# Kernel tuning notes

Measured on AMD Instinct MI355X. Metric: run time of the kernel, lower is better.

The kernel has to match this reference:

```python
import jax, jax.numpy as jnp
import numpy as np


def setup_inputs() -> dict:
    key = jax.random.key(0)
    k_x, k_g, k_fc, k_pj = jax.random.split(key, 4)
    B, T, C, H, E = 4, 2048, 1024, 2048, 8
    n_layer = 12
    x = jax.random.normal(k_x, (B, T, C), dtype=jnp.float32)
    w_gate = 0.02 * jax.random.normal(k_g, (C, E), dtype=jnp.float32)
    w_fc = 0.02 * jax.random.normal(k_fc, (C, H, E), dtype=jnp.float32)
    w_proj = (0.02 * (2 * n_layer) ** -0.5) * jax.random.normal(k_pj, (H, C, E), dtype=jnp.float32)
    return {"x": x, "w_gate": w_gate, "w_fc": w_fc, "w_proj": w_proj, "top_k": 2}


def reference(x, w_gate, w_fc, w_proj, top_k):
    # x: (B,T,C); w_gate: (C,E); w_fc: (C,H,E); w_proj: (H,C,E)
    E = w_gate.shape[-1]
    gate = jnp.einsum('btc,ce->bte', x, w_gate)                  # gating logits
    top_vals, top_idx = jax.lax.top_k(gate, top_k)               # (B,T,K) — raw logits used as combine weights (as in source)
    # Per-expert combine weight: sum_k top_val_k * onehot(idx_k) — zero for unselected experts.
    # This is mathematically identical to gathering the K expert weight slices per token
    # (the source's gather+einsum) but avoids the (B,T,C,H,K) weight blowup.
    onehot = jax.nn.one_hot(top_idx, E, dtype=x.dtype)           # (B,T,K,E)
    w_e = jnp.einsum('btk,btke->bte', top_vals, onehot)          # (B,T,E)
    h = jax.nn.silu(jnp.einsum('btc,che->bthe', x, w_fc))        # (B,T,H,E)
    o = jnp.einsum('bthe,bte,hce->btc', h, w_e, w_proj)          # weighted expert combine
    return o
```

## Files before the change

### kernel.cpp

```cpp
#include <hip/hip_runtime.h>
#include <hip/hip_bf16.h>


#define NTOK 8192
#define CD   1024
#define HD   2048
#define NE   8
#define NSLOT 16384
#define MTILES 20

typedef short  short4_t  __attribute__((ext_vector_type(4)));
typedef short  short8_t  __attribute__((ext_vector_type(8)));
typedef __bf16 bf16x8_t  __attribute__((ext_vector_type(8)));
typedef float  f32x4_t   __attribute__((ext_vector_type(4)));

struct FragArg {
  short8_t v;
  __device__ operator short8_t() const { return v; }
  __device__ operator bf16x8_t() const { return __builtin_bit_cast(bf16x8_t, v); }
};

static __device__ __forceinline__ float b2f(unsigned short u) {
  union { float f; unsigned int i; } w; w.i = ((unsigned int)u) << 16; return w.f;
}
static __device__ __forceinline__ unsigned short f2b(float f) {
  unsigned int u = __float_as_uint(f);
  u += 0x7fffu + ((u >> 16) & 1u);
  return (unsigned short)(u >> 16);
}
static __device__ __forceinline__ void gl2lds16(const void* g, void* l) {
  __builtin_amdgcn_global_load_lds((__attribute__((address_space(1))) void*)g,
                                   (__attribute__((address_space(3))) void*)l,
                                   16, 0, 0);
}
static __device__ __forceinline__ int swz(int row, int kc) {
  return row * 4 + (kc ^ ((row >> 1) & 3));
}

#define GATE_BLOCKS (NTOK / 4)
__global__ __launch_bounds__(256) void prep_kernel(
    const float* __restrict__ x, const float* __restrict__ wg,
    const float* __restrict__ wfc, const float* __restrict__ wpj,
    unsigned short* __restrict__ xb,
    unsigned short* __restrict__ wfcp, unsigned short* __restrict__ wpjp,
    int* __restrict__ tok_e, float* __restrict__ tok_v,
    int* __restrict__ g_counts)
{
  __shared__ __align__(16) unsigned short lds[NE * 32 * 40];
  __shared__ int hist[NE];
  int t = threadIdx.x;

  if (blockIdx.x < GATE_BLOCKS) {
    if (t < NE) hist[t] = 0;
    __syncthreads();
    int wv = t >> 6, lane = t & 63;
    int tk = blockIdx.x * 4 + wv;
    const float* xr = x + (size_t)tk * CD;
    unsigned short* xbr = xb + (size_t)tk * CD;
    float acc[NE] = {0, 0, 0, 0, 0, 0, 0, 0};
    #pragma unroll
    for (int jj = 0; jj < 4; ++jj) {
      int c0 = (lane + 64 * jj) * 4;
      float4 xv = *(const float4*)(xr + c0);
      short4_t ob;
      ob[0] = (short)f2b(xv.x); ob[1] = (short)f2b(xv.y);
      ob[2] = (short)f2b(xv.z); ob[3] = (short)f2b(xv.w);
      *(short4_t*)(xbr + c0) = ob;
      #pragma unroll
      for (int j = 0; j < 4; ++j) {
        float xf = (j == 0) ? xv.x : (j == 1) ? xv.y : (j == 2) ? xv.z : xv.w;
        const float* wr = wg + (size_t)(c0 + j) * NE;
        float4 w0 = *(const float4*)wr;
        float4 w1 = *(const float4*)(wr + 4);
        acc[0] += xf * w0.x; acc[1] += xf * w0.y;
        acc[2] += xf * w0.z; acc[3] += xf * w0.w;
        acc[4] += xf * w1.x; acc[5] += xf * w1.y;
        acc[6] += xf * w1.z; acc[7] += xf * w1.w;
      }
    }
    #pragma unroll
    for (int off = 32; off >= 1; off >>= 1)
      #pragma unroll
      for (int e = 0; e < NE; ++e) acc[e] += __shfl_down(acc[e], off, 64);
    if (lane == 0) {
      float v1 = -3.0e38f, v2 = -3.0e38f; int i1 = 0, i2 = 1;
      #pragma unroll
      for (int e = 0; e < NE; ++e) {
        float g = acc[e];
        if (g > v1) { v2 = v1; i2 = i1; v1 = g; i1 = e; }
        else if (g > v2) { v2 = g; i2 = e; }
      }
      tok_e[tk * 2] = i1; tok_e[tk * 2 + 1] = i2;
      tok_v[tk * 2] = v1; tok_v[tk * 2 + 1] = v2;
      atomicAdd(&hist[i1], 1); atomicAdd(&hist[i2], 1);
    }
    __syncthreads();
    if (t < NE && hist[t] > 0) atomicAdd(&g_counts[t], hist[t]);
  } else {
    int pid = blockIdx.x - GATE_BLOCKS;
    int tensor = pid >> 11;
    int rem = pid & 2047;
    int bx = rem & 63, by = rem >> 6;
    const float* in; unsigned short* out; int D0, D1, b0, b1;
    if (tensor == 0) { in = wfc; out = wfcp; D0 = CD; D1 = HD;
                       b1 = bx * 32; b0 = by * 32; }
    else             { in = wpj; out = wpjp; D0 = HD; D1 = CD;
                       b1 = by * 32; b0 = bx * 32; }
    int d1i = t & 31, d0q = t >> 5;
    #pragma unroll
    for (int r = 0; r < 4; ++r) {
      int d0i = d0q * 4 + r;
      const float* src = in + ((size_t)(b0 + d0i) * D1 + (b1 + d1i)) * NE;
      float4 v0 = *(const float4*)src;
      float4 v1 = *(const float4*)(src + 4);
      unsigned short* dst0 = &lds[d1i * 40 + d0i];
      dst0[0 * 32 * 40] = f2b(v0.x);
      dst0[1 * 32 * 40] = f2b(v0.y);
      dst0[2 * 32 * 40] = f2b(v0.z);
      dst0[3 * 32 * 40] = f2b(v0.w);
      dst0[4 * 32 * 40] = f2b(v1.x);
      dst0[5 * 32 * 40] = f2b(v1.y);
      dst0[6 * 32 * 40] = f2b(v1.z);
      dst0[7 * 32 * 40] = f2b(v1.w);
    }
    __syncthreads();
    int dchunk = t & 3, d1w = (t >> 2) & 31, ehalf = t >> 7;
    #pragma unroll
    for (int p = 0; p < 4; ++p) {
      int e = ehalf + 2 * p;
      short8_t v = *(const short8_t*)&lds[e * 32 * 40 + d1w * 40 + dchunk * 8];
      *(short8_t*)(out + ((size_t)e * D1 + (b1 + d1w)) * D0 + b0 + dchunk * 8) = v;
    }
  }
}

__global__ __launch_bounds__(256) void scatter_kernel(
    const int* __restrict__ tok_e, const float* __restrict__ tok_v,
    const int* __restrict__ g_counts, int* __restrict__ g_cursor,
    int* __restrict__ g_base,
    int* __restrict__ bucket_tok, float* __restrict__ bucket_v,
    int* __restrict__ slot_of)
{
  int gid = blockIdx.x * 256 + threadIdx.x;
  int lane = threadIdx.x & 63;
  int base[NE];
  { int o = 0;
    #pragma unroll
    for (int e = 0; e < NE; ++e) { base[e] = o; o += g_counts[e]; } }
  int e = tok_e[gid];
  unsigned long long lanebit = 1ull << lane;
  int pos = 0;
  #pragma unroll
  for (int ee = 0; ee < NE; ++ee) {
    unsigned long long m = __ballot(e == ee);
    if (e == ee) {
      int leader = __ffsll((long long)m) - 1;
      int cnt = __popcll(m);
      int start = 0;
      if (lane == leader) start = atomicAdd(&g_cursor[ee], cnt);
      start = __shfl(start, leader, 64);
      pos = start + __popcll(m & (lanebit - 1));
    }
  }
  int sl = base[e] + pos;
  bucket_tok[sl] = gid >> 1;
  bucket_v[sl]   = tok_v[gid];
  slot_of[gid]   = sl;
  if (gid < NE) g_base[gid] = base[gid];
}

__global__ __launch_bounds__(256) void gemm1_kernel(
    const unsigned short* __restrict__ xb, const unsigned short* __restrict__ wfcp,
    const int* __restrict__ g_counts, const int* __restrict__ g_base,
    const int* __restrict__ bucket_tok, const float* __restrict__ bucket_v,
    unsigned short* __restrict__ hbuf)
{
  int id = blockIdx.x;
  int xcd = id & 7;
  int r = id >> 3;
  int nt = r & 15;
  int g = (r >> 4) * 8 + xcd;
  int e = g / MTILES, mt = g % MTILES;

  int cnt = g_counts[e];
  int m0 = mt * 128;
  if (m0 >= cnt) return;
  int base = g_base[e];
  int n0 = nt * 128;

  __shared__ __align__(16) unsigned short lsA[128 * 32];
  __shared__ __align__(16) unsigned short lsB[128 * 32];
  __shared__ int   s_tok[128];
  __shared__ float s_v[128];

  int t = threadIdx.x;
  if (t < 128) {
    int ok = (m0 + t) < cnt;
    s_tok[t] = ok ? bucket_tok[base + m0 + t] : 0;
    s_v[t]   = ok ? bucket_v[base + m0 + t] : 0.0f;
  }
  __syncthreads();

  int slot = t & 3;
  int r0 = t >> 2, r1 = r0 + 64;
  int gc0 = slot ^ ((r0 >> 1) & 3);
  int gc1 = slot ^ ((r1 >> 1) & 3);
  const unsigned short* gA0 = xb + (size_t)s_tok[r0] * CD + gc0 * 8;
  const unsigned short* gA1 = xb + (size_t)s_tok[r1] * CD + gc1 * 8;
  const unsigned short* gB0 = wfcp + ((size_t)e * HD + n0 + r0) * CD + gc0 * 8;
  const unsigned short* gB1 = wfcp + ((size_t)e * HD + n0 + r1) * CD + gc1 * 8;
  unsigned short* lA0 = &lsA[(size_t)t * 8];
  unsigned short* lA1 = &lsA[(size_t)(256 + t) * 8];
  unsigned short* lB0 = &lsB[(size_t)t * 8];
  unsigned short* lB1 = &lsB[(size_t)(256 + t) * 8];

  int lane = t & 63, wv = t >> 6;
  int wm = (wv & 1) * 64, wn = (wv >> 1) * 64;
  int ml = lane & 15, kq = lane >> 4;

  f32x4_t acc[4][4];
  #pragma unroll
  for (int i = 0; i < 4; ++i)
    #pragma unroll
    for (int j = 0; j < 4; ++j) acc[i][j] = (f32x4_t){0.f, 0.f, 0.f, 0.f};

  for (int k0 = 0; k0 < CD; k0 += 32) {
    __syncthreads();
    gl2lds16(gA0 + k0, lA0);
    gl2lds16(gA1 + k0, lA1);
    gl2lds16(gB0 + k0, lB0);
    gl2lds16(gB1 + k0, lB1);
    __syncthreads();
    short8_t af[4], bfr[4];
    #pragma unroll
    for (int i = 0; i < 4; ++i) {
      af[i]  = *(const short8_t*)&lsA[swz(wm + i * 16 + ml, kq) * 8];
      bfr[i] = *(const short8_t*)&lsB[swz(wn + i * 16 + ml, kq) * 8];
    }
    #pragma unroll
    for (int i = 0; i < 4; ++i)
      #pragma unroll
      for (int j = 0; j < 4; ++j)
        acc[i][j] = __builtin_amdgcn_mfma_f32_16x16x32_bf16(
            FragArg{af[i]}, FragArg{bfr[j]}, acc[i][j], 0, 0, 0);
  }

  #pragma unroll
  for (int i = 0; i < 4; ++i) {
    int rb = wm + i * 16 + kq * 4;
    #pragma unroll
    for (int r2 = 0; r2 < 4; ++r2) {
      int row = rb + r2;
      if (m0 + row < cnt) {
        float v = s_v[row];
        size_t ro = (size_t)(base + m0 + row) * HD + n0;
        #pragma unroll
        for (int j = 0; j < 4; ++j) {
          float z = acc[i][j][r2];
          float val = v * (z / (1.0f + __expf(-z)));
          hbuf[ro + wn + j * 16 + ml] = f2b(val);
        }
      }
    }
  }
}

__global__ __launch_bounds__(256) void gemm2_kernel(
    const unsigned short* __restrict__ hbuf, const unsigned short* __restrict__ wpjp,
    const int* __restrict__ g_counts, const int* __restrict__ g_base,
    unsigned short* __restrict__ oslot)
{
  int id = blockIdx.x;
  int xcd = id & 7;
  int r = id >> 3;
  int nt = r & 7;
  int g = (r >> 3) * 8 + xcd;
  int e = g / MTILES, mt = g % MTILES;

  int cnt = g_counts[e];
  int m0 = mt * 128;
  if (m0 >= cnt) return;
  int base = g_base[e];
  int n0 = nt * 128;

  __shared__ __align__(16) unsigned short lsA[128 * 32];
  __shared__ __align__(16) unsigned short lsB[128 * 32];

  int t = threadIdx.x;
  int slot = t & 3;
  int r0 = t >> 2, r1 = r0 + 64;
  int gc0 = slot ^ ((r0 >> 1) & 3);
  int gc1 = slot ^ ((r1 >> 1) & 3);
  const unsigned short* gA0 = hbuf + (size_t)(base + m0 + r0) * HD + gc0 * 8;
  const unsigned short* gA1 = hbuf + (size_t)(base + m0 + r1) * HD + gc1 * 8;
  const unsigned short* gB0 = wpjp + ((size_t)e * CD + n0 + r0) * HD + gc0 * 8;
  const unsigned short* gB1 = wpjp + ((size_t)e * CD + n0 + r1) * HD + gc1 * 8;
  unsigned short* lA0 = &lsA[(size_t)t * 8];
  unsigned short* lA1 = &lsA[(size_t)(256 + t) * 8];
  unsigned short* lB0 = &lsB[(size_t)t * 8];
  unsigned short* lB1 = &lsB[(size_t)(256 + t) * 8];

  int lane = t & 63, wv = t >> 6;
  int wm = (wv & 1) * 64, wn = (wv >> 1) * 64;
  int ml = lane & 15, kq = lane >> 4;

  f32x4_t acc[4][4];
  #pragma unroll
  for (int i = 0; i < 4; ++i)
    #pragma unroll
    for (int j = 0; j < 4; ++j) acc[i][j] = (f32x4_t){0.f, 0.f, 0.f, 0.f};

  for (int k0 = 0; k0 < HD; k0 += 32) {
    __syncthreads();
    gl2lds16(gA0 + k0, lA0);
    gl2lds16(gA1 + k0, lA1);
    gl2lds16(gB0 + k0, lB0);
    gl2lds16(gB1 + k0, lB1);
    __syncthreads();
    short8_t af[4], bfr[4];
    #pragma unroll
    for (int i = 0; i < 4; ++i) {
      af[i]  = *(const short8_t*)&lsA[swz(wm + i * 16 + ml, kq) * 8];
      bfr[i] = *(const short8_t*)&lsB[swz(wn + i * 16 + ml, kq) * 8];
    }
    #pragma unroll
    for (int i = 0; i < 4; ++i)
      #pragma unroll
      for (int j = 0; j < 4; ++j)
        acc[i][j] = __builtin_amdgcn_mfma_f32_16x16x32_bf16(
            FragArg{af[i]}, FragArg{bfr[j]}, acc[i][j], 0, 0, 0);
  }

  #pragma unroll
  for (int i = 0; i < 4; ++i) {
    int rb = wm + i * 16 + kq * 4;
    #pragma unroll
    for (int r2 = 0; r2 < 4; ++r2) {
      int row = rb + r2;
      if (m0 + row < cnt) {
        size_t ro = (size_t)(base + m0 + row) * CD + n0;
        #pragma unroll
        for (int j = 0; j < 4; ++j)
          oslot[ro + wn + j * 16 + ml] = f2b(acc[i][j][r2]);
      }
    }
  }
}

__global__ __launch_bounds__(256) void combine_kernel(
    const unsigned short* __restrict__ oslot, const int* __restrict__ slot_of,
    float* __restrict__ out)
{
  int gid = blockIdx.x * 256 + threadIdx.x;
  int tk = gid >> 7;
  int ch = (gid & 127) * 8;
  int s0 = slot_of[tk * 2], s1 = slot_of[tk * 2 + 1];
  short8_t a = *(const short8_t*)(oslot + (size_t)s0 * CD + ch);
  short8_t b = *(const short8_t*)(oslot + (size_t)s1 * CD + ch);
  float* op = out + (size_t)tk * CD + ch;
  float4 o0, o1;
  o0.x = b2f((unsigned short)a[0]) + b2f((unsigned short)b[0]);
  o0.y = b2f((unsigned short)a[1]) + b2f((unsigned short)b[1]);
  o0.z = b2f((unsigned short)a[2]) + b2f((unsigned short)b[2]);
  o0.w = b2f((unsigned short)a[3]) + b2f((unsigned short)b[3]);
  o1.x = b2f((unsigned short)a[4]) + b2f((unsigned short)b[4]);
  o1.y = b2f((unsigned short)a[5]) + b2f((unsigned short)b[5]);
  o1.z = b2f((unsigned short)a[6]) + b2f((unsigned short)b[6]);
  o1.w = b2f((unsigned short)a[7]) + b2f((unsigned short)b[7]);
  *(float4*)op = o0;
  *(float4*)(op + 4) = o1;
}

extern "C" void kernel_launch(void* const* d_in, const int* in_sizes, int n_in,
                              void* d_out, int out_size, void* d_ws, size_t ws_size,
                              hipStream_t stream)
{
  const float* x   = (const float*)d_in[0];
  const float* wg  = (const float*)d_in[1];
  const float* wfc = (const float*)d_in[2];
  const float* wpj = (const float*)d_in[3];
  float* out = (float*)d_out;

  char* w = (char*)d_ws;
  unsigned short* wfcp  = (unsigned short*)w; w += (size_t)NE * HD * CD * 2;
  unsigned short* wpjp  = (unsigned short*)w; w += (size_t)NE * CD * HD * 2;
  unsigned short* xb    = (unsigned short*)w; w += (size_t)NTOK * CD * 2;
  unsigned short* hbuf  = (unsigned short*)w; w += (size_t)NSLOT * HD * 2;
  unsigned short* oslot = (unsigned short*)w; w += (size_t)NSLOT * CD * 2;
  int*   tok_e      = (int*)w;   w += NSLOT * 4;
  float* tok_v      = (float*)w; w += NSLOT * 4;
  int*   slot_of    = (int*)w;   w += NSLOT * 4;
  int*   bucket_tok = (int*)w;   w += NSLOT * 4;
  float* bucket_v   = (float*)w; w += NSLOT * 4;
  int*   g_counts   = (int*)w;   w += NE * 4;
  int*   g_cursor   = (int*)w;   w += NE * 4;
  int*   g_base     = (int*)w;   w += 256;

  hipMemsetAsync(g_counts, 0, 2 * NE * sizeof(int), stream);
  prep_kernel<<<GATE_BLOCKS + 4096, 256, 0, stream>>>(
      x, wg, wfc, wpj, xb, wfcp, wpjp, tok_e, tok_v, g_counts);
  scatter_kernel<<<NSLOT / 256, 256, 0, stream>>>(
      tok_e, tok_v, g_counts, g_cursor, g_base, bucket_tok, bucket_v, slot_of);
  gemm1_kernel<<<(HD / 128) * MTILES * NE, 256, 0, stream>>>(
      xb, wfcp, g_counts, g_base, bucket_tok, bucket_v, hbuf);
  gemm2_kernel<<<(CD / 128) * MTILES * NE, 256, 0, stream>>>(
      hbuf, wpjp, g_counts, g_base, oslot);
  combine_kernel<<<(NTOK * CD / 8) / 256, 256, 0, stream>>>(oslot, slot_of, out);
}
```

Before: 466.4 us.

## Double K-tile depth to 64 and remap grid so expert follows XCD index

Both expert GEMM kernels now stage 64-wide K slices in LDS instead of 32, with an 8-way XOR swizzle and a per-wave load mapping. This halves the number of barrier pairs per output tile and gives two MFMA sub-steps per sync. Block indexing also changes so the expert id is taken from the low three bits of the block id, tying each expert to one XCD so its weights stay in that die's L2. LDS use doubles per block, which may lower occupancy, and per-XCD load now depends on how many tokens each expert receives.

```diff
diff --git a/kernel.cpp b/kernel.cpp
--- a/kernel.cpp
+++ b/kernel.cpp
@@ -8,6 +8,7 @@
 #define NE   8
 #define NSLOT 16384
 #define MTILES 20
+#define BK   64
 
 typedef short  short4_t  __attribute__((ext_vector_type(4)));
 typedef short  short8_t  __attribute__((ext_vector_type(8)));
@@ -32,9 +33,6 @@
   __builtin_amdgcn_global_load_lds((__attribute__((address_space(1))) void*)g,
                                    (__attribute__((address_space(3))) void*)l,
                                    16, 0, 0);
-}
-static __device__ __forceinline__ int swz(int row, int kc) {
-  return row * 4 + (kc ^ ((row >> 1) & 3));
 }
 
 #define GATE_BLOCKS (NTOK / 4)
@@ -176,11 +174,10 @@
     unsigned short* __restrict__ hbuf)
 {
   int id = blockIdx.x;
-  int xcd = id & 7;
+  int e = id & 7;
   int r = id >> 3;
   int nt = r & 15;
-  int g = (r >> 4) * 8 + xcd;
-  int e = g / MTILES, mt = g % MTILES;
+  int mt = r >> 4;
 
   int cnt = g_counts[e];
   int m0 = mt * 128;
@@ -188,8 +185,8 @@
   int base = g_base[e];
   int n0 = nt * 128;
 
-  __shared__ __align__(16) unsigned short lsA[128 * 32];
-  __shared__ __align__(16) unsigned short lsB[128 * 32];
+  __shared__ __align__(16) unsigned short lsA[128 * BK];
+  __shared__ __align__(16) unsigned short lsB[128 * BK];
   __shared__ int   s_tok[128];
   __shared__ float s_v[128];
 
@@ -201,20 +198,20 @@
   }
   __syncthreads();
 
-  int slot = t & 3;
-  int r0 = t >> 2, r1 = r0 + 64;
-  int gc0 = slot ^ ((r0 >> 1) & 3);
-  int gc1 = slot ^ ((r1 >> 1) & 3);
-  const unsigned short* gA0 = xb + (size_t)s_tok[r0] * CD + gc0 * 8;
-  const unsigned short* gA1 = xb + (size_t)s_tok[r1] * CD + gc1 * 8;
-  const unsigned short* gB0 = wfcp + ((size_t)e * HD + n0 + r0) * CD + gc0 * 8;
-  const unsigned short* gB1 = wfcp + ((size_t)e * HD + n0 + r1) * CD + gc1 * 8;
-  unsigned short* lA0 = &lsA[(size_t)t * 8];
-  unsigned short* lA1 = &lsA[(size_t)(256 + t) * 8];
-  unsigned short* lB0 = &lsB[(size_t)t * 8];
-  unsigned short* lB1 = &lsB[(size_t)(256 + t) * 8];
-
   int lane = t & 63, wv = t >> 6;
+  int subrow = lane >> 3, kc = lane & 7;
+  const unsigned short* pA[4]; const unsigned short* pB[4];
+  unsigned short* dA[4]; unsigned short* dB[4];
+  #pragma unroll
+  for (int p = 0; p < 4; ++p) {
+    int rr = p * 32 + wv * 8 + subrow;
+    int gc = kc ^ ((rr >> 1) & 7);
+    pA[p] = xb + (size_t)s_tok[rr] * CD + gc * 8;
+    pB[p] = wfcp + ((size_t)e * HD + n0 + rr) * CD + gc * 8;
+    dA[p] = &lsA[(p * 32 + wv * 8) * BK];
+    dB[p] = &lsB[(p * 32 + wv * 8) * BK];
+  }
+
   int wm = (wv & 1) * 64, wn = (wv >> 1) * 64;
   int ml = lane & 15, kq = lane >> 4;
 
@@ -224,25 +221,31 @@
     #pragma unroll
     for (int j = 0; j < 4; ++j) acc[i][j] = (f32x4_t){0.f, 0.f, 0.f, 0.f};
 
-  for (int k0 = 0; k0 < CD; k0 += 32) {
-    __syncthreads();
-    gl2lds16(gA0 + k0, lA0);
-    gl2lds16(gA1 + k0, lA1);
-    gl2lds16(gB0 + k0, lB0);
-    gl2lds16(gB1 + k0, lB1);
-    __syncthreads();
-    short8_t af[4], bfr[4];
-    #pragma unroll
-    for (int i = 0; i < 4; ++i) {
-      af[i]  = *(const short8_t*)&lsA[swz(wm + i * 16 + ml, kq) * 8];
-      bfr[i] = *(const short8_t*)&lsB[swz(wn + i * 16 + ml, kq) * 8];
-    }
-    #pragma unroll
-    for (int i = 0; i < 4; ++i)
-      #pragma unroll
-      for (int j = 0; j < 4; ++j)
-        acc[i][j] = __builtin_amdgcn_mfma_f32_16x16x32_bf16(
-            FragArg{af[i]}, FragArg{bfr[j]}, acc[i][j], 0, 0, 0);
+  for (int k0 = 0; k0 < CD; k0 += BK) {
+    __syncthreads();
+    #pragma unroll
+    for (int p = 0; p < 4; ++p) {
+      gl2lds16(pA[p], dA[p]); pA[p] += BK;
+      gl2lds16(pB[p], dB[p]); pB[p] += BK;
+    }
+    __syncthreads();
+    #pragma unroll
+    for (int s = 0; s < 2; ++s) {
+      short8_t af[4], bfr[4];
+      #pragma unroll
+      for (int i = 0; i < 4; ++i) {
+        int ar = wm + i * 16 + ml;
+        af[i]  = *(const short8_t*)&lsA[ar * BK + (((s * 4 + kq) ^ ((ar >> 1) & 7)) * 8)];
+        int br = wn + i * 16 + ml;
+        bfr[i] = *(const short8_t*)&lsB[br * BK + (((s * 4 + kq) ^ ((br >> 1) & 7)) * 8)];
+      }
+      #pragma unroll
+      for (int i = 0; i < 4; ++i)
+        #pragma unroll
+        for (int j = 0; j < 4; ++j)
+          acc[i][j] = __builtin_amdgcn_mfma_f32_16x16x32_bf16(
+              FragArg{af[i]}, FragArg{bfr[j]}, acc[i][j], 0, 0, 0);
+    }
   }
 
   #pragma unroll
@@ -271,11 +274,10 @@
     unsigned short* __restrict__ oslot)
 {
   int id = blockIdx.x;
-  int xcd = id & 7;
+  int e = id & 7;
   int r = id >> 3;
   int nt = r & 7;
-  int g = (r >> 3) * 8 + xcd;
-  int e = g / MTILES, mt = g % MTILES;
+  int mt = r >> 3;
 
   int cnt = g_counts[e];
   int m0 = mt * 128;
@@ -283,24 +285,24 @@
   int base = g_base[e];
   int n0 = nt * 128;
 
-  __shared__ __align__(16) unsigned short lsA[128 * 32];
-  __shared__ __align__(16) unsigned short lsB[128 * 32];
+  __shared__ __align__(16) unsigned short lsA[128 * BK];
+  __shared__ __align__(16) unsigned short lsB[128 * BK];
 
   int t = threadIdx.x;
-  int slot = t & 3;
-  int r0 = t >> 2, r1 = r0 + 64;
-  int gc0 = slot ^ ((r0 >> 1) & 3);
-  int gc1 = slot ^ ((r1 >> 1) & 3);
-  const unsigned short* gA0 = hbuf + (size_t)(base + m0 + r0) * HD + gc0 * 8;
-  const unsigned short* gA1 = hbuf + (size_t)(base + m0 + r1) * HD + gc1 * 8;
-  const unsigned short* gB0 = wpjp + ((size_t)e * CD + n0 + r0) * HD + gc0 * 8;
-  const unsigned short* gB1 = wpjp + ((size_t)e * CD + n0 + r1) * HD + gc1 * 8;
-  unsigned short* lA0 = &lsA[(size_t)t * 8];
-  unsigned short* lA1 = &lsA[(size_t)(256 + t) * 8];
-  unsigned short* lB0 = &lsB[(size_t)t * 8];
-  unsigned short* lB1 = &lsB[(size_t)(256 + t) * 8];
-
   int lane = t & 63, wv = t >> 6;
+  int subrow = lane >> 3, kc = lane & 7;
+  const unsigned short* pA[4]; const unsigned short* pB[4];
+  unsigned short* dA[4]; unsigned short* dB[4];
+  #pragma unroll
+  for (int p = 0; p < 4; ++p) {
+    int rr = p * 32 + wv * 8 + subrow;
+    int gc = kc ^ ((rr >> 1) & 7);
+    pA[p] = hbuf + ((size_t)(base + m0 + rr)) * HD + gc * 8;
+    pB[p] = wpjp + ((size_t)e * CD + n0 + rr) * HD + gc * 8;
+    dA[p] = &lsA[(p * 32 + wv * 8) * BK];
+    dB[p] = &lsB[(p * 32 + wv * 8) * BK];
+  }
+
   int wm = (wv & 1) * 64, wn = (wv >> 1) * 64;
   int ml = lane & 15, kq = lane >> 4;
 
@@ -310,25 +312,31 @@
     #pragma unroll
     for (int j = 0; j < 4; ++j) acc[i][j] = (f32x4_t){0.f, 0.f, 0.f, 0.f};
 
-  for (int k0 = 0; k0 < HD; k0 += 32) {
-    __syncthreads();
-    gl2lds16(gA0 + k0, lA0);
-    gl2lds16(gA1 + k0, lA1);
-    gl2lds16(gB0 + k0, lB0);
-    gl2lds16(gB1 + k0, lB1);
-    __syncthreads();
-    short8_t af[4], bfr[4];
-    #pragma unroll
-    for (int i = 0; i < 4; ++i) {
-      af[i]  = *(const short8_t*)&lsA[swz(wm + i * 16 + ml, kq) * 8];
-      bfr[i] = *(const short8_t*)&lsB[swz(wn + i * 16 + ml, kq) * 8];
-    }
-    #pragma unroll
-    for (int i = 0; i < 4; ++i)
-      #pragma unroll
-      for (int j = 0; j < 4; ++j)
-        acc[i][j] = __builtin_amdgcn_mfma_f32_16x16x32_bf16(
-            FragArg{af[i]}, FragArg{bfr[j]}, acc[i][j], 0, 0, 0);
+  for (int k0 = 0; k0 < HD; k0 += BK) {
+    __syncthreads();
+    #pragma unroll
+    for (int p = 0; p < 4; ++p) {
+      gl2lds16(pA[p], dA[p]); pA[p] += BK;
+      gl2lds16(pB[p], dB[p]); pB[p] += BK;
+    }
+    __syncthreads();
+    #pragma unroll
+    for (int s = 0; s < 2; ++s) {
+      short8_t af[4], bfr[4];
+      #pragma unroll
+      for (int i = 0; i < 4; ++i) {
+        int ar = wm + i * 16 + ml;
+        af[i]  = *(const short8_t*)&lsA[ar * BK + (((s * 4 + kq) ^ ((ar >> 1) & 7)) * 8)];
+        int br = wn + i * 16 + ml;
+        bfr[i] = *(const short8_t*)&lsB[br * BK + (((s * 4 + kq) ^ ((br >> 1) & 7)) * 8)];
+      }
+      #pragma unroll
+      for (int i = 0; i < 4; ++i)
+        #pragma unroll
+        for (int j = 0; j < 4; ++j)
+          acc[i][j] = __builtin_amdgcn_mfma_f32_16x16x32_bf16(
+              FragArg{af[i]}, FragArg{bfr[j]}, acc[i][j], 0, 0, 0);
+    }
   }
 
   #pragma unroll
```

Measured after the change: 454.3 us. 1.03x faster.
